# Kernel tuning notes

Hardware: AMD Instinct MI355X
Metric: run time of the kernel (lower is better)

## Reference

```python
import jax, jax.numpy as jnp
import numpy as np

H, W = 72, 128            # raster_h, raster_w
THICK = 0.03              # raster_thickness
SHARP = 80.0              # sigmoid sharpness
NRS = 64                  # match_resample_n
BIG = 1e9                 # finite stand-in for inf (grad-safe)
PTS_W, TAN_W, CURV_W, OVL_W = 5.0, 1.0, 0.5, 2.0


def _grid_xy():
    ys = jnp.linspace(0.0, 1.0, H)
    xs = jnp.linspace(0.0, 1.0, W)
    yy, xx = jnp.meshgrid(ys, xs, indexing='ij')
    return jnp.stack([xx, yy], -1).reshape(-1, 2)  # [H*W, 2]


def _prepare_mask(vis):
    # visibility -> per-point mask; curves with <2 visible points fall back to all-visible
    raw = vis > 0.5
    fallback = raw.sum(-1) < 2
    return jnp.where(fallback[:, None], 1.0, raw.astype(jnp.float32))  # [m, p]


def _resample(curves, pm, num):
    # arc-length resampling of [m, p, 2] polylines to [m, num, 2]
    m, p, _ = curves.shape
    seg_valid = pm[:, :-1] * pm[:, 1:]
    seg_len = jnp.linalg.norm(curves[:, 1:] - curves[:, :-1], axis=-1) * seg_valid
    cum = jnp.concatenate([jnp.zeros((m, 1), curves.dtype), jnp.cumsum(seg_len, -1)], -1)  # [m, p]
    total = cum[:, -1]
    base_t = jnp.linspace(0.0, 1.0, num)
    t = base_t[None] * total[:, None]  # [m, num]
    idx = jax.vmap(lambda c, tt: jnp.searchsorted(c, tt, side='right'))(cum, t) - 1
    idx = jnp.clip(idx, 0, p - 2)
    left = jnp.take_along_axis(curves[:, :-1], idx[..., None], axis=1)
    right = jnp.take_along_axis(curves[:, 1:], idx[..., None], axis=1)
    lt = jnp.take_along_axis(cum[:, :-1], idx, axis=1)
    rt = jnp.take_along_axis(cum[:, 1:], idx, axis=1)
    alpha = ((t - lt) / jnp.maximum(rt - lt, 1e-8))[..., None]
    out = left + alpha * (right - left)
    return jnp.where((total < 1e-8)[:, None, None], curves[:, :1, :], out)


def _tangents(pts):
    # central-difference unit tangents, [m, n, 2]
    fwd = jnp.concatenate([pts[:, 1:2] - pts[:, 0:1],
                           pts[:, 2:] - pts[:, :-2],
                           pts[:, -1:] - pts[:, -2:-1]], axis=1)
    return fwd / jnp.maximum(jnp.linalg.norm(fwd, axis=-1, keepdims=True), 1e-8)


def _pt2poly(A, B):
    # mean over resampled points of A of min point-to-segment distance to polyline B
    # A: [qa, r, 2], B: [qb, r, 2] -> [qa, qb]
    seg_a = B[:, :-1]
    ab = B[:, 1:] - seg_a
    denom = jnp.maximum((ab * ab).sum(-1), 1e-8)  # [qb, s]
    ap = A[:, None, :, None, :] - seg_a[None, :, None]           # [qa, qb, r, s, 2]
    t = jnp.clip((ap * ab[None, :, None]).sum(-1) / denom[None, :, None], 0.0, 1.0)
    proj = seg_a[None, :, None] + t[..., None] * ab[None, :, None]
    dist = jnp.linalg.norm(A[:, None, :, None, :] - proj, axis=-1)  # [qa, qb, r, s]
    return dist.min(-1).mean(-1)


def _smooth_l1(x, y):
    d = jnp.abs(x - y)
    return jnp.where(d < 1.0, 0.5 * d * d, d - 0.5)


def _soft_mask(curves, pm, grid):
    # soft rasterization of polylines: [m, p, 2] -> [m, H*W]
    seg_a = curves[:, :-1]
    ab = curves[:, 1:] - seg_a
    denom = jnp.maximum((ab * ab).sum(-1), 1e-8)          # [m, s]
    seg_valid = (pm[:, :-1] * pm[:, 1:]) > 0.5
    ap = grid[None, :, None, :] - seg_a[:, None]          # [m, HW, s, 2]
    t = jnp.clip((ap * ab[:, None]).sum(-1) / denom[:, None], 0.0, 1.0)
    proj = seg_a[:, None] + t[..., None] * ab[:, None]
    dist = jnp.linalg.norm(grid[None, :, None, :] - proj, axis=-1)  # [m, HW, s]
    dist = jnp.where(seg_valid[:, None], dist, BIG)
    min_dist = dist.min(-1)
    # fallback to nearest visible point when a curve has no valid segment
    no_valid = ~seg_valid.any(-1)
    pd = jnp.linalg.norm(grid[None, :, None, :] - curves[:, None], axis=-1)  # [m, HW, p]
    pd = jnp.where(pm[:, None] > 0.5, pd, BIG)
    min_dist = jnp.where(no_valid[:, None], pd.min(-1), min_dist)
    return jax.nn.sigmoid((THICK - min_dist) * SHARP)


def _cost_single(pred, gtp, gtv, grid):
    gt_pm = _prepare_mask(gtv)
    ones_pm = jnp.ones(pred.shape[:2], pred.dtype)
    pred_rs = _resample(pred, ones_pm, NRS)
    gt_rs = _resample(gtp, gt_pm, NRS)
    d_pg = _pt2poly(pred_rs, gt_rs)
    d_gp = _pt2poly(gt_rs, pred_rs).T
    sym = 0.5 * (d_pg + d_gp)                                   # [Q, M]
    pt = _tangents(pred_rs)
    gt_t = _tangents(gt_rs)
    tan = 1.0 - jnp.abs((pt[:, None] * gt_t[None]).sum(-1)).mean(-1)
    ps = pred_rs[:, 2:] - 2 * pred_rs[:, 1:-1] + pred_rs[:, :-2]
    gs = gt_rs[:, 2:] - 2 * gt_rs[:, 1:-1] + gt_rs[:, :-2]
    curv = _smooth_l1(ps[:, None], gs[None]).mean((-1, -2))
    pmask = _soft_mask(pred, ones_pm, grid)                     # [Q, HW]
    gmask = _soft_mask(gtp, gt_pm, grid)                        # [M, HW]
    inter = jnp.minimum(pmask[:, None], gmask[None]).sum(-1)
    union = jnp.maximum(pmask[:, None], gmask[None]).sum(-1)
    overlap = 1.0 - inter / (union + 1e-8)
    return PTS_W * sym + TAN_W * tan + CURV_W * curv + OVL_W * overlap


def setup_inputs() -> dict:
    key = jax.random.key(0)
    k1, k2, k3, k4 = jax.random.split(key, 4)
    return {
        'pred_pts': jax.random.uniform(k1, (2, 40, 24, 2), jnp.float32),
        'gt_pts': jax.random.uniform(k2, (2, 24, 24, 2), jnp.float32),
        'gt_vis': jax.random.uniform(k3, (2, 24, 24), jnp.float32),
        'gt_exist': jax.random.uniform(k4, (2, 24), jnp.float32),
    }


def reference(pred_pts, gt_pts, gt_vis, gt_exist):
    grid = _grid_xy()
    cost = jax.vmap(lambda p, g, v: _cost_single(p, g, v, grid))(pred_pts, gt_pts, gt_vis)
    # zero out columns for non-existent GT lanes (original skips them via boolean indexing)
    return cost * (gt_exist > 0.5).astype(cost.dtype)[:, None, :]  # [B, Q, M]
```

## Files before the change

### kernel.cpp

```cpp
#include <hip/hip_runtime.h>
#include <math.h>

#define Hh 72
#define Ww 128
#define HW (Hh*Ww)
#define NP 24
#define NSEG (NP-1)
#define Mp 40
#define Ng 24
#define Bb 2
#define NRS 64
#define THICKc 0.03f
#define SHARPc 80.0f

__global__ __launch_bounds__(64) void k_resample(
    const float* __restrict__ pred,
    const float* __restrict__ gt,
    const float* __restrict__ vis,
    float* __restrict__ predRS,
    float* __restrict__ gtRS,
    float* __restrict__ gtPM)
{
    int blk = blockIdx.x;
    int b = blk / (Mp + Ng);
    int c = blk % (Mp + Ng);
    bool isPred = (c < Mp);
    int tid = threadIdx.x;

    __shared__ float qx[NP], qy[NP], pm[NP], cum[NP];
    __shared__ float s_total;

    const float* src = isPred ? pred + (size_t)(b * Mp + c) * NP * 2
                              : gt   + (size_t)(b * Ng + (c - Mp)) * NP * 2;
    if (tid < NP) {
        float2 v = ((const float2*)src)[tid];
        qx[tid] = v.x;
        qy[tid] = v.y;
        pm[tid] = isPred ? 1.0f
                         : ((vis[(b * Ng + (c - Mp)) * NP + tid] > 0.5f) ? 1.0f : 0.0f);
    }
    __syncthreads();
    if (tid == 0) {
        if (!isPred) {
            float s = 0.0f;
            for (int p = 0; p < NP; p++) s += pm[p];
            if (s < 2.0f)
                for (int p = 0; p < NP; p++) pm[p] = 1.0f;
        }
        float acc = 0.0f;
        cum[0] = 0.0f;
        for (int s = 0; s < NSEG; s++) {
            float dx = qx[s + 1] - qx[s], dy = qy[s + 1] - qy[s];
            float sl = sqrtf(dx * dx + dy * dy) * (pm[s] * pm[s + 1]);
            acc += sl;
            cum[s + 1] = acc;
        }
        s_total = acc;
    }
    __syncthreads();
    if (!isPred && tid < NP) gtPM[(b * Ng + (c - Mp)) * NP + tid] = pm[tid];

    float total = s_total;
    float t = ((float)tid / 63.0f) * total;
    int cnt = 0;
    for (int p = 0; p < NP; p++) cnt += (cum[p] <= t) ? 1 : 0;
    int idx = cnt - 1;
    idx = (idx < 0) ? 0 : ((idx > NP - 2) ? NP - 2 : idx);
    float lt = cum[idx], rt = cum[idx + 1];
    float alpha = (t - lt) / fmaxf(rt - lt, 1e-8f);
    float ox = qx[idx] + alpha * (qx[idx + 1] - qx[idx]);
    float oy = qy[idx] + alpha * (qy[idx + 1] - qy[idx]);
    if (total < 1e-8f) { ox = qx[0]; oy = qy[0]; }
    float* dst = isPred ? predRS + (size_t)(b * Mp + c) * NRS * 2
                        : gtRS   + (size_t)(b * Ng + (c - Mp)) * NRS * 2;
    dst[tid * 2 + 0] = ox;
    dst[tid * 2 + 1] = oy;
}

__global__ __launch_bounds__(256) void k_softmask(
    const float* __restrict__ pred,
    const float* __restrict__ gt,
    const float* __restrict__ gtPM,
    float* __restrict__ pmask,
    float* __restrict__ gmask)
{
    int c = blockIdx.y;
    int b = c / (Mp + Ng);
    int cc = c % (Mp + Ng);
    bool isPred = (cc < Mp);
    int g = blockIdx.x * blockDim.x + threadIdx.x;

    __shared__ float qx[NP], qy[NP], pm[NP];
    __shared__ float sax[NSEG], say[NSEG], sabx[NSEG], saby[NSEG], sinv[NSEG], svld[NSEG];
    if (threadIdx.x < NP) {
        const float* src = isPred ? pred + (size_t)(b * Mp + cc) * NP * 2
                                  : gt   + (size_t)(b * Ng + (cc - Mp)) * NP * 2;
        float2 v = ((const float2*)src)[threadIdx.x];
        qx[threadIdx.x] = v.x;
        qy[threadIdx.x] = v.y;
        pm[threadIdx.x] = isPred ? 1.0f : gtPM[(b * Ng + (cc - Mp)) * NP + threadIdx.x];
    }
    __syncthreads();
    if (threadIdx.x < NSEG) {
        int s = threadIdx.x;
        float ax = qx[s], ay = qy[s];
        float abx = qx[s + 1] - ax, aby = qy[s + 1] - ay;
        sax[s] = ax; say[s] = ay; sabx[s] = abx; saby[s] = aby;
        sinv[s] = 1.0f / fmaxf(abx * abx + aby * aby, 1e-8f);
        svld[s] = (pm[s] * pm[s + 1] > 0.5f) ? 1.0f : 0.0f;
    }
    __syncthreads();

    float gx = (float)(g & (Ww - 1)) * (1.0f / 127.0f);
    float gy = (float)(g >> 7) * (1.0f / 71.0f);

    float best2 = 1e30f;
    bool anyValid = false;
    for (int s = 0; s < NSEG; s++) {
        if (svld[s] > 0.5f) {
            anyValid = true;
            float ax = sax[s], ay = say[s];
            float abx = sabx[s], aby = saby[s];
            float t = ((gx - ax) * abx + (gy - ay) * aby) * sinv[s];
            t = fminf(fmaxf(t, 0.0f), 1.0f);
            float dx = gx - (ax + t * abx), dy = gy - (ay + t * aby);
            best2 = fminf(best2, dx * dx + dy * dy);
        }
    }
    float mind;
    if (anyValid) {
        mind = sqrtf(best2);
    } else {
        float b2 = 1e30f;
        for (int p = 0; p < NP; p++) {
            if (pm[p] > 0.5f) {
                float dx = gx - qx[p], dy = gy - qy[p];
                b2 = fminf(b2, dx * dx + dy * dy);
            }
        }
        mind = sqrtf(b2);
    }
    float x = (THICKc - mind) * SHARPc;
    float mval = 1.0f / (1.0f + __expf(-x));
    if (isPred) pmask[(size_t)(b * Mp + cc) * HW + g] = mval;
    else        gmask[(size_t)(b * Ng + (cc - Mp)) * HW + g] = mval;
}

__global__ __launch_bounds__(256) void k_cost(
    const float* __restrict__ predRS,
    const float* __restrict__ gtRS,
    const float* __restrict__ pmask,
    const float* __restrict__ gmask,
    const float* __restrict__ gtExist,
    float* __restrict__ out)
{
    int pair = blockIdx.x;
    int j = pair % Ng;
    int i = (pair / Ng) % Mp;
    int b = pair / (Ng * Mp);
    int tid = threadIdx.x;
    int lane = tid & 63, wid = tid >> 6;

    __shared__ float px[NRS], py[NRS], gxr[NRS], gyr[NRS];
    __shared__ float pmin[4], psp[4], psq[4];

    if (tid < NRS) {
        px[tid]  = predRS[((size_t)(b * Mp + i) * NRS + tid) * 2 + 0];
        py[tid]  = predRS[((size_t)(b * Mp + i) * NRS + tid) * 2 + 1];
        gxr[tid] = gtRS[((size_t)(b * Ng + j) * NRS + tid) * 2 + 0];
        gyr[tid] = gtRS[((size_t)(b * Ng + j) * NRS + tid) * 2 + 1];
    }
    __syncthreads();

    const float4* pm4 = (const float4*)(pmask + (size_t)(b * Mp + i) * HW);
    const float4* gm4 = (const float4*)(gmask + (size_t)(b * Ng + j) * HW);
    float smin = 0.0f, sp = 0.0f, sq = 0.0f;
    for (int g = tid; g < HW / 4; g += 256) {
        float4 p = pm4[g], q = gm4[g];
        smin += fminf(p.x, q.x) + fminf(p.y, q.y) + fminf(p.z, q.z) + fminf(p.w, q.w);
        sp   += p.x + p.y + p.z + p.w;
        sq   += q.x + q.y + q.z + q.w;
    }

    float symv = 0.0f, tanv = 0.0f, curvv = 0.0f;
    if (wid == 0) {
        float p0x = px[lane], p0y = py[lane];
        float bst = 1e30f;
        for (int s = 0; s < NRS - 1; s++) {
            float ax = gxr[s], ay = gyr[s];
            float abx = gxr[s + 1] - ax, aby = gyr[s + 1] - ay;
            float denom = fmaxf(abx * abx + aby * aby, 1e-8f);
            float t = ((p0x - ax) * abx + (p0y - ay) * aby) / denom;
            t = fminf(fmaxf(t, 0.0f), 1.0f);
            float dx = p0x - (ax + t * abx), dy = p0y - (ay + t * aby);
            bst = fminf(bst, dx * dx + dy * dy);
        }
        float dpg = sqrtf(bst);
        float q0x = gxr[lane], q0y = gyr[lane];
        bst = 1e30f;
        for (int s = 0; s < NRS - 1; s++) {
            float ax = px[s], ay = py[s];
            float abx = px[s + 1] - ax, aby = py[s + 1] - ay;
            float denom = fmaxf(abx * abx + aby * aby, 1e-8f);
            float t = ((q0x - ax) * abx + (q0y - ay) * aby) / denom;
            t = fminf(fmaxf(t, 0.0f), 1.0f);
            float dx = q0x - (ax + t * abx), dy = q0y - (ay + t * aby);
            bst = fminf(bst, dx * dx + dy * dy);
        }
        float dgp = sqrtf(bst);
        symv = 0.5f * (dpg + dgp);

        int kp = (lane == NRS - 1) ? NRS - 1 : lane + 1;
        int km = (lane == 0) ? 0 : lane - 1;
        float tx = px[kp] - px[km], ty = py[kp] - py[km];
        float nrm = fmaxf(sqrtf(tx * tx + ty * ty), 1e-8f);
        tx /= nrm; ty /= nrm;
        float gtx = gxr[kp] - gxr[km], gty = gyr[kp] - gyr[km];
        float nrm2 = fmaxf(sqrtf(gtx * gtx + gty * gty), 1e-8f);
        gtx /= nrm2; gty /= nrm2;
        tanv = fabsf(tx * gtx + ty * gty);

        if (lane < NRS - 2) {
            float psx = px[lane + 2] - 2.0f * px[lane + 1] + px[lane];
            float psy = py[lane + 2] - 2.0f * py[lane + 1] + py[lane];
            float gsx = gxr[lane + 2] - 2.0f * gxr[lane + 1] + gxr[lane];
            float gsy = gyr[lane + 2] - 2.0f * gyr[lane + 1] + gyr[lane];
            float d1 = fabsf(psx - gsx);
            float d2 = fabsf(psy - gsy);
            float c1 = (d1 < 1.0f) ? 0.5f * d1 * d1 : d1 - 0.5f;
            float c2 = (d2 < 1.0f) ? 0.5f * d2 * d2 : d2 - 0.5f;
            curvv = c1 + c2;
        }
    }

    for (int off = 32; off > 0; off >>= 1) {
        smin += __shfl_down(smin, off);
        sp   += __shfl_down(sp, off);
        sq   += __shfl_down(sq, off);
    }
    if (lane == 0) { pmin[wid] = smin; psp[wid] = sp; psq[wid] = sq; }
    if (wid == 0) {
        for (int off = 32; off > 0; off >>= 1) {
            symv  += __shfl_down(symv,  off);
            tanv  += __shfl_down(tanv,  off);
            curvv += __shfl_down(curvv, off);
        }
    }
    __syncthreads();

    if (tid == 0) {
        float Smin = pmin[0] + pmin[1] + pmin[2] + pmin[3];
        float Sp   = psp[0] + psp[1] + psp[2] + psp[3];
        float Sq   = psq[0] + psq[1] + psq[2] + psq[3];
        float Smax = Sp + Sq - Smin;
        float overlap = 1.0f - Smin / (Smax + 1e-8f);
        float sym  = symv * (1.0f / 64.0f);
        float tanl = 1.0f - tanv * (1.0f / 64.0f);
        float curv = curvv * (1.0f / 124.0f);
        float cost = 5.0f * sym + 1.0f * tanl + 0.5f * curv + 2.0f * overlap;
        float e = (gtExist[b * Ng + j] > 0.5f) ? 1.0f : 0.0f;
        out[(size_t)(b * Mp + i) * Ng + j] = cost * e;
    }
}

extern "C" void kernel_launch(void* const* d_in, const int* in_sizes, int n_in,
                              void* d_out, int out_size, void* d_ws, size_t ws_size,
                              hipStream_t stream) {
    (void)in_sizes; (void)n_in; (void)out_size; (void)ws_size;
    const float* pred  = (const float*)d_in[0];
    const float* gt    = (const float*)d_in[1];
    const float* vis   = (const float*)d_in[2];
    const float* exist = (const float*)d_in[3];

    float* ws      = (float*)d_ws;
    float* predRS  = ws;
    float* gtRS    = predRS + (size_t)Bb * Mp * NRS * 2;
    float* gtPM    = gtRS   + (size_t)Bb * Ng * NRS * 2;
    float* pmask   = gtPM   + (size_t)Bb * Ng * NP;
    float* gmask   = pmask  + (size_t)Bb * Mp * HW;
    float* outp    = (float*)d_out;

    hipLaunchKernelGGL(k_resample, dim3(Bb * (Mp + Ng)), dim3(64), 0, stream,
                       pred, gt, vis, predRS, gtRS, gtPM);
    hipLaunchKernelGGL(k_softmask, dim3(HW / 256, Bb * (Mp + Ng)), dim3(256), 0, stream,
                       pred, gt, gtPM, pmask, gmask);
    hipLaunchKernelGGL(k_cost, dim3(Bb * Mp * Ng), dim3(256), 0, stream,
                       predRS, gtRS, pmask, gmask, exist, outp);
}
```

Measured before the change: 99.71 us.

## Precompute compacted segment data and tile cost kernel over 2x2 pred/GT pairs

The prep kernel now builds a compacted list of valid segments per curve, with the projection coefficients already folded in. The soft-mask kernel then loops only over those segments using FMAs and no branches. The cost kernel handles a 2x2 tile of (pred, GT) pairs per block, so each mask row is loaded once and reused for two intersections. The chamfer, tangent and curvature terms are spread across all four waves instead of one. This cuts global mask traffic, but each block now does more register-heavy work and there are fewer blocks (480 instead of 1920).

Measured after the change: 100.8 us. Within noise of the previous version (+1.0%).

```diff
diff --git a/kernel.cpp b/kernel.cpp
--- a/kernel.cpp
+++ b/kernel.cpp
@@ -12,32 +12,35 @@
 #define NRS 64
 #define THICKc 0.03f
 #define SHARPc 80.0f
-
-__global__ __launch_bounds__(64) void k_resample(
+#define NCURV (Bb*(Mp+Ng))
+
+__global__ __launch_bounds__(64) void k_prep(
     const float* __restrict__ pred,
     const float* __restrict__ gt,
     const float* __restrict__ vis,
     float* __restrict__ predRS,
     float* __restrict__ gtRS,
-    float* __restrict__ gtPM)
+    float* __restrict__ segData,
+    int*   __restrict__ segCount)
 {
-    int blk = blockIdx.x;
-    int b = blk / (Mp + Ng);
-    int c = blk % (Mp + Ng);
-    bool isPred = (c < Mp);
+    int c = blockIdx.x;
+    bool isPred = (c < Bb * Mp);
+    int b   = isPred ? (c / Mp) : ((c - Bb * Mp) / Ng);
+    int idx = isPred ? (c % Mp) : ((c - Bb * Mp) % Ng);
+    const float* src = isPred ? pred + (size_t)(b * Mp + idx) * NP * 2
+                              : gt   + (size_t)(b * Ng + idx) * NP * 2;
     int tid = threadIdx.x;
 
     __shared__ float qx[NP], qy[NP], pm[NP], cum[NP];
+    __shared__ int   sidx[NP];
+    __shared__ int   s_mode;
     __shared__ float s_total;
 
-    const float* src = isPred ? pred + (size_t)(b * Mp + c) * NP * 2
-                              : gt   + (size_t)(b * Ng + (c - Mp)) * NP * 2;
     if (tid < NP) {
         float2 v = ((const float2*)src)[tid];
-        qx[tid] = v.x;
-        qy[tid] = v.y;
+        qx[tid] = v.x; qy[tid] = v.y;
         pm[tid] = isPred ? 1.0f
-                         : ((vis[(b * Ng + (c - Mp)) * NP + tid] > 0.5f) ? 1.0f : 0.0f);
+                         : ((vis[(b * Ng + idx) * NP + tid] > 0.5f) ? 1.0f : 0.0f);
     }
     __syncthreads();
     if (tid == 0) {
@@ -51,215 +54,216 @@
         cum[0] = 0.0f;
         for (int s = 0; s < NSEG; s++) {
             float dx = qx[s + 1] - qx[s], dy = qy[s + 1] - qy[s];
-            float sl = sqrtf(dx * dx + dy * dy) * (pm[s] * pm[s + 1]);
-            acc += sl;
+            acc += sqrtf(dx * dx + dy * dy) * (pm[s] * pm[s + 1]);
             cum[s + 1] = acc;
         }
         s_total = acc;
-    }
-    __syncthreads();
-    if (!isPred && tid < NP) gtPM[(b * Ng + (c - Mp)) * NP + tid] = pm[tid];
+        int n = 0;
+        for (int s = 0; s < NSEG; s++) sidx[s] = (pm[s] * pm[s + 1] > 0.5f) ? n++ : -1;
+        if (n > 0) {
+            s_mode = 0;
+        } else {
+            s_mode = 1;
+            for (int p = 0; p < NP; p++) sidx[p] = (pm[p] > 0.5f) ? n++ : -1;
+        }
+        segCount[c] = n;
+    }
+    __syncthreads();
+
+    if (s_mode == 0) {
+        if (tid < NSEG && sidx[tid] >= 0) {
+            float ax = qx[tid], ay = qy[tid];
+            float abx = qx[tid + 1] - ax, aby = qy[tid + 1] - ay;
+            float inv = 1.0f / fmaxf(abx * abx + aby * aby, 1e-8f);
+            float* r = segData + ((size_t)c * NP + sidx[tid]) * 8;
+            r[0] = ax;  r[1] = ay;  r[2] = abx;       r[3] = aby;
+            r[4] = abx * inv; r[5] = aby * inv; r[6] = (ax * abx + ay * aby) * inv; r[7] = 0.f;
+        }
+    } else {
+        if (tid < NP && sidx[tid] >= 0) {
+            float* r = segData + ((size_t)c * NP + sidx[tid]) * 8;
+            r[0] = qx[tid]; r[1] = qy[tid]; r[2] = 0.f; r[3] = 0.f;
+            r[4] = 0.f;     r[5] = 0.f;     r[6] = 0.f; r[7] = 0.f;
+        }
+    }
 
     float total = s_total;
     float t = ((float)tid / 63.0f) * total;
     int cnt = 0;
     for (int p = 0; p < NP; p++) cnt += (cum[p] <= t) ? 1 : 0;
-    int idx = cnt - 1;
-    idx = (idx < 0) ? 0 : ((idx > NP - 2) ? NP - 2 : idx);
-    float lt = cum[idx], rt = cum[idx + 1];
+    int id2 = cnt - 1;
+    id2 = (id2 < 0) ? 0 : ((id2 > NP - 2) ? NP - 2 : id2);
+    float lt = cum[id2], rt = cum[id2 + 1];
     float alpha = (t - lt) / fmaxf(rt - lt, 1e-8f);
-    float ox = qx[idx] + alpha * (qx[idx + 1] - qx[idx]);
-    float oy = qy[idx] + alpha * (qy[idx + 1] - qy[idx]);
+    float ox = qx[id2] + alpha * (qx[id2 + 1] - qx[id2]);
+    float oy = qy[id2] + alpha * (qy[id2 + 1] - qy[id2]);
     if (total < 1e-8f) { ox = qx[0]; oy = qy[0]; }
-    float* dst = isPred ? predRS + (size_t)(b * Mp + c) * NRS * 2
-                        : gtRS   + (size_t)(b * Ng + (c - Mp)) * NRS * 2;
-    dst[tid * 2 + 0] = ox;
-    dst[tid * 2 + 1] = oy;
+    float* dst = isPred ? predRS + ((size_t)(b * Mp + idx) * NRS + tid) * 2
+                        : gtRS   + ((size_t)(b * Ng + idx) * NRS + tid) * 2;
+    dst[0] = ox; dst[1] = oy;
 }
 
 __global__ __launch_bounds__(256) void k_softmask(
-    const float* __restrict__ pred,
-    const float* __restrict__ gt,
-    const float* __restrict__ gtPM,
-    float* __restrict__ pmask,
-    float* __restrict__ gmask)
+    const float* __restrict__ segData,
+    const int*   __restrict__ segCount,
+    float* __restrict__ maskAll)
 {
     int c = blockIdx.y;
-    int b = c / (Mp + Ng);
-    int cc = c % (Mp + Ng);
-    bool isPred = (cc < Mp);
-    int g = blockIdx.x * blockDim.x + threadIdx.x;
-
-    __shared__ float qx[NP], qy[NP], pm[NP];
-    __shared__ float sax[NSEG], say[NSEG], sabx[NSEG], saby[NSEG], sinv[NSEG], svld[NSEG];
-    if (threadIdx.x < NP) {
-        const float* src = isPred ? pred + (size_t)(b * Mp + cc) * NP * 2
-                                  : gt   + (size_t)(b * Ng + (cc - Mp)) * NP * 2;
-        float2 v = ((const float2*)src)[threadIdx.x];
-        qx[threadIdx.x] = v.x;
-        qy[threadIdx.x] = v.y;
-        pm[threadIdx.x] = isPred ? 1.0f : gtPM[(b * Ng + (cc - Mp)) * NP + threadIdx.x];
-    }
-    __syncthreads();
-    if (threadIdx.x < NSEG) {
-        int s = threadIdx.x;
-        float ax = qx[s], ay = qy[s];
-        float abx = qx[s + 1] - ax, aby = qy[s + 1] - ay;
-        sax[s] = ax; say[s] = ay; sabx[s] = abx; saby[s] = aby;
-        sinv[s] = 1.0f / fmaxf(abx * abx + aby * aby, 1e-8f);
-        svld[s] = (pm[s] * pm[s + 1] > 0.5f) ? 1.0f : 0.0f;
-    }
-    __syncthreads();
+    int g = blockIdx.x * 256 + threadIdx.x;
+    int n = segCount[c];
+    const float4* sd = (const float4*)(segData + (size_t)c * NP * 8);
 
     float gx = (float)(g & (Ww - 1)) * (1.0f / 127.0f);
-    float gy = (float)(g >> 7) * (1.0f / 71.0f);
+    float gy = (float)(g >> 7)       * (1.0f / 71.0f);
 
     float best2 = 1e30f;
-    bool anyValid = false;
-    for (int s = 0; s < NSEG; s++) {
-        if (svld[s] > 0.5f) {
-            anyValid = true;
-            float ax = sax[s], ay = say[s];
-            float abx = sabx[s], aby = saby[s];
-            float t = ((gx - ax) * abx + (gy - ay) * aby) * sinv[s];
-            t = fminf(fmaxf(t, 0.0f), 1.0f);
-            float dx = gx - (ax + t * abx), dy = gy - (ay + t * aby);
-            best2 = fminf(best2, dx * dx + dy * dy);
-        }
-    }
-    float mind;
-    if (anyValid) {
-        mind = sqrtf(best2);
-    } else {
-        float b2 = 1e30f;
-        for (int p = 0; p < NP; p++) {
-            if (pm[p] > 0.5f) {
-                float dx = gx - qx[p], dy = gy - qy[p];
-                b2 = fminf(b2, dx * dx + dy * dy);
-            }
-        }
-        mind = sqrtf(b2);
-    }
-    float x = (THICKc - mind) * SHARPc;
-    float mval = 1.0f / (1.0f + __expf(-x));
-    if (isPred) pmask[(size_t)(b * Mp + cc) * HW + g] = mval;
-    else        gmask[(size_t)(b * Ng + (cc - Mp)) * HW + g] = mval;
+    for (int s = 0; s < n; s++) {
+        float4 A  = sd[s * 2];
+        float4 Bv = sd[s * 2 + 1];
+        float t = fmaf(gx, Bv.x, fmaf(gy, Bv.y, -Bv.z));
+        t = fminf(fmaxf(t, 0.0f), 1.0f);
+        float dx = gx - fmaf(t, A.z, A.x);
+        float dy = gy - fmaf(t, A.w, A.y);
+        best2 = fminf(best2, fmaf(dx, dx, dy * dy));
+    }
+    float mind = sqrtf(best2);
+    float mval = 1.0f / (1.0f + __expf((mind - THICKc) * SHARPc));
+    maskAll[(size_t)c * HW + g] = mval;
 }
 
 __global__ __launch_bounds__(256) void k_cost(
     const float* __restrict__ predRS,
     const float* __restrict__ gtRS,
-    const float* __restrict__ pmask,
-    const float* __restrict__ gmask,
+    const float* __restrict__ maskAll,
     const float* __restrict__ gtExist,
     float* __restrict__ out)
 {
-    int pair = blockIdx.x;
-    int j = pair % Ng;
-    int i = (pair / Ng) % Mp;
-    int b = pair / (Ng * Mp);
+    int blk = blockIdx.x;
+    int tj = blk % 12;
+    int ti = (blk / 12) % 20;
+    int b  = blk / (12 * 20);
+    int i0 = ti * 2, j0 = tj * 2;
     int tid = threadIdx.x;
-    int lane = tid & 63, wid = tid >> 6;
-
-    __shared__ float px[NRS], py[NRS], gxr[NRS], gyr[NRS];
-    __shared__ float pmin[4], psp[4], psq[4];
-
-    if (tid < NRS) {
-        px[tid]  = predRS[((size_t)(b * Mp + i) * NRS + tid) * 2 + 0];
-        py[tid]  = predRS[((size_t)(b * Mp + i) * NRS + tid) * 2 + 1];
-        gxr[tid] = gtRS[((size_t)(b * Ng + j) * NRS + tid) * 2 + 0];
-        gyr[tid] = gtRS[((size_t)(b * Ng + j) * NRS + tid) * 2 + 1];
-    }
-    __syncthreads();
-
-    const float4* pm4 = (const float4*)(pmask + (size_t)(b * Mp + i) * HW);
-    const float4* gm4 = (const float4*)(gmask + (size_t)(b * Ng + j) * HW);
-    float smin = 0.0f, sp = 0.0f, sq = 0.0f;
+    int lane = tid & 63, w = tid >> 6;
+
+    __shared__ float sPx[2][NRS], sPy[2][NRS], sGx[2][NRS], sGy[2][NRS];
+    __shared__ float partA[4][8];
+    __shared__ float cham[4][3];
+
+    {
+        int ci = tid >> 6, pt = tid & 63;
+        if (ci < 2) {
+            float2 v = ((const float2*)predRS)[(b * Mp + i0 + ci) * NRS + pt];
+            sPx[ci][pt] = v.x; sPy[ci][pt] = v.y;
+        } else {
+            int cj = ci - 2;
+            float2 v = ((const float2*)gtRS)[(b * Ng + j0 + cj) * NRS + pt];
+            sGx[cj][pt] = v.x; sGy[cj][pt] = v.y;
+        }
+    }
+    __syncthreads();
+
+    const float4* P0 = (const float4*)(maskAll + (size_t)(b * Mp + i0)     * HW);
+    const float4* P1 = (const float4*)(maskAll + (size_t)(b * Mp + i0 + 1) * HW);
+    const float4* Q0 = (const float4*)(maskAll + (size_t)(Bb * Mp + b * Ng + j0)     * HW);
+    const float4* Q1 = (const float4*)(maskAll + (size_t)(Bb * Mp + b * Ng + j0 + 1) * HW);
+    float sm00 = 0, sm01 = 0, sm10 = 0, sm11 = 0;
+    float sp0 = 0, sp1 = 0, sq0 = 0, sq1 = 0;
     for (int g = tid; g < HW / 4; g += 256) {
-        float4 p = pm4[g], q = gm4[g];
-        smin += fminf(p.x, q.x) + fminf(p.y, q.y) + fminf(p.z, q.z) + fminf(p.w, q.w);
-        sp   += p.x + p.y + p.z + p.w;
-        sq   += q.x + q.y + q.z + q.w;
-    }
-
-    float symv = 0.0f, tanv = 0.0f, curvv = 0.0f;
-    if (wid == 0) {
-        float p0x = px[lane], p0y = py[lane];
-        float bst = 1e30f;
+        float4 p0 = P0[g], p1 = P1[g], q0 = Q0[g], q1 = Q1[g];
+        sp0 += p0.x + p0.y + p0.z + p0.w;
+        sp1 += p1.x + p1.y + p1.z + p1.w;
+        sq0 += q0.x + q0.y + q0.z + q0.w;
+        sq1 += q1.x + q1.y + q1.z + q1.w;
+        sm00 += fminf(p0.x,q0.x) + fminf(p0.y,q0.y) + fminf(p0.z,q0.z) + fminf(p0.w,q0.w);
+        sm01 += fminf(p0.x,q1.x) + fminf(p0.y,q1.y) + fminf(p0.z,q1.z) + fminf(p0.w,q1.w);
+        sm10 += fminf(p1.x,q0.x) + fminf(p1.y,q0.y) + fminf(p1.z,q0.z) + fminf(p1.w,q0.w);
+        sm11 += fminf(p1.x,q1.x) + fminf(p1.y,q1.y) + fminf(p1.z,q1.z) + fminf(p1.w,q1.w);
+    }
+    for (int off = 32; off > 0; off >>= 1) {
+        sm00 += __shfl_down(sm00, off); sm01 += __shfl_down(sm01, off);
+        sm10 += __shfl_down(sm10, off); sm11 += __shfl_down(sm11, off);
+        sp0  += __shfl_down(sp0,  off); sp1  += __shfl_down(sp1,  off);
+        sq0  += __shfl_down(sq0,  off); sq1  += __shfl_down(sq1,  off);
+    }
+    if (lane == 0) {
+        partA[w][0] = sm00; partA[w][1] = sm01; partA[w][2] = sm10; partA[w][3] = sm11;
+        partA[w][4] = sp0;  partA[w][5] = sp1;  partA[w][6] = sq0;  partA[w][7] = sq1;
+    }
+
+    {
+        int a = w >> 1, cj = w & 1;
+        const float* PX = sPx[a];  const float* PY = sPy[a];
+        const float* GX = sGx[cj]; const float* GY = sGy[cj];
+        float p0x = PX[lane], p0y = PY[lane];
+        float q0x = GX[lane], q0y = GY[lane];
+        float b1 = 1e30f, b2 = 1e30f;
         for (int s = 0; s < NRS - 1; s++) {
-            float ax = gxr[s], ay = gyr[s];
-            float abx = gxr[s + 1] - ax, aby = gyr[s + 1] - ay;
-            float denom = fmaxf(abx * abx + aby * aby, 1e-8f);
-            float t = ((p0x - ax) * abx + (p0y - ay) * aby) / denom;
-            t = fminf(fmaxf(t, 0.0f), 1.0f);
-            float dx = p0x - (ax + t * abx), dy = p0y - (ay + t * aby);
-            bst = fminf(bst, dx * dx + dy * dy);
-        }
-        float dpg = sqrtf(bst);
-        float q0x = gxr[lane], q0y = gyr[lane];
-        bst = 1e30f;
-        for (int s = 0; s < NRS - 1; s++) {
-            float ax = px[s], ay = py[s];
-            float abx = px[s + 1] - ax, aby = py[s + 1] - ay;
-            float denom = fmaxf(abx * abx + aby * aby, 1e-8f);
-            float t = ((q0x - ax) * abx + (q0y - ay) * aby) / denom;
-            t = fminf(fmaxf(t, 0.0f), 1.0f);
-            float dx = q0x - (ax + t * abx), dy = q0y - (ay + t * aby);
-            bst = fminf(bst, dx * dx + dy * dy);
-        }
-        float dgp = sqrtf(bst);
-        symv = 0.5f * (dpg + dgp);
+            {
+                float ax = GX[s], ay = GY[s];
+                float abx = GX[s + 1] - ax, aby = GY[s + 1] - ay;
+                float denom = fmaxf(abx * abx + aby * aby, 1e-8f);
+                float t = ((p0x - ax) * abx + (p0y - ay) * aby) / denom;
+                t = fminf(fmaxf(t, 0.0f), 1.0f);
+                float dx = p0x - (ax + t * abx), dy = p0y - (ay + t * aby);
+                b1 = fminf(b1, dx * dx + dy * dy);
+            }
+            {
+                float ax = PX[s], ay = PY[s];
+                float abx = PX[s + 1] - ax, aby = PY[s + 1] - ay;
+                float denom = fmaxf(abx * abx + aby * aby, 1e-8f);
+                float t = ((q0x - ax) * abx + (q0y - ay) * aby) / denom;
+                t = fminf(fmaxf(t, 0.0f), 1.0f);
+                float dx = q0x - (ax + t * abx), dy = q0y - (ay + t * aby);
+                b2 = fminf(b2, dx * dx + dy * dy);
+            }
+        }
+        float symv = 0.5f * (sqrtf(b1) + sqrtf(b2));
 
         int kp = (lane == NRS - 1) ? NRS - 1 : lane + 1;
         int km = (lane == 0) ? 0 : lane - 1;
-        float tx = px[kp] - px[km], ty = py[kp] - py[km];
+        float tx = PX[kp] - PX[km], ty = PY[kp] - PY[km];
         float nrm = fmaxf(sqrtf(tx * tx + ty * ty), 1e-8f);
         tx /= nrm; ty /= nrm;
-        float gtx = gxr[kp] - gxr[km], gty = gyr[kp] - gyr[km];
+        float gtx = GX[kp] - GX[km], gty = GY[kp] - GY[km];
         float nrm2 = fmaxf(sqrtf(gtx * gtx + gty * gty), 1e-8f);
         gtx /= nrm2; gty /= nrm2;
-        tanv = fabsf(tx * gtx + ty * gty);
-
+        float tanv = fabsf(tx * gtx + ty * gty);
+
+        float curvv = 0.0f;
         if (lane < NRS - 2) {
-            float psx = px[lane + 2] - 2.0f * px[lane + 1] + px[lane];
-            float psy = py[lane + 2] - 2.0f * py[lane + 1] + py[lane];
-            float gsx = gxr[lane + 2] - 2.0f * gxr[lane + 1] + gxr[lane];
-            float gsy = gyr[lane + 2] - 2.0f * gyr[lane + 1] + gyr[lane];
+            float psx = PX[lane + 2] - 2.0f * PX[lane + 1] + PX[lane];
+            float psy = PY[lane + 2] - 2.0f * PY[lane + 1] + PY[lane];
+            float gsx = GX[lane + 2] - 2.0f * GX[lane + 1] + GX[lane];
+            float gsy = GY[lane + 2] - 2.0f * GY[lane + 1] + GY[lane];
             float d1 = fabsf(psx - gsx);
             float d2 = fabsf(psy - gsy);
             float c1 = (d1 < 1.0f) ? 0.5f * d1 * d1 : d1 - 0.5f;
             float c2 = (d2 < 1.0f) ? 0.5f * d2 * d2 : d2 - 0.5f;
             curvv = c1 + c2;
         }
-    }
-
-    for (int off = 32; off > 0; off >>= 1) {
-        smin += __shfl_down(smin, off);
-        sp   += __shfl_down(sp, off);
-        sq   += __shfl_down(sq, off);
-    }
-    if (lane == 0) { pmin[wid] = smin; psp[wid] = sp; psq[wid] = sq; }
-    if (wid == 0) {
         for (int off = 32; off > 0; off >>= 1) {
             symv  += __shfl_down(symv,  off);
             tanv  += __shfl_down(tanv,  off);
             curvv += __shfl_down(curvv, off);
         }
-    }
-    __syncthreads();
-
-    if (tid == 0) {
-        float Smin = pmin[0] + pmin[1] + pmin[2] + pmin[3];
-        float Sp   = psp[0] + psp[1] + psp[2] + psp[3];
-        float Sq   = psq[0] + psq[1] + psq[2] + psq[3];
+        if (lane == 0) { cham[w][0] = symv; cham[w][1] = tanv; cham[w][2] = curvv; }
+    }
+    __syncthreads();
+
+    if (tid < 4) {
+        int a2 = tid >> 1, c2 = tid & 1;
+        float Smin = partA[0][tid] + partA[1][tid] + partA[2][tid] + partA[3][tid];
+        float Sp = partA[0][4 + a2] + partA[1][4 + a2] + partA[2][4 + a2] + partA[3][4 + a2];
+        float Sq = partA[0][6 + c2] + partA[1][6 + c2] + partA[2][6 + c2] + partA[3][6 + c2];
         float Smax = Sp + Sq - Smin;
         float overlap = 1.0f - Smin / (Smax + 1e-8f);
-        float sym  = symv * (1.0f / 64.0f);
-        float tanl = 1.0f - tanv * (1.0f / 64.0f);
-        float curv = curvv * (1.0f / 124.0f);
+        float sym  = cham[tid][0] * (1.0f / 64.0f);
+        float tanl = 1.0f - cham[tid][1] * (1.0f / 64.0f);
+        float curv = cham[tid][2] * (1.0f / 124.0f);
         float cost = 5.0f * sym + 1.0f * tanl + 0.5f * curv + 2.0f * overlap;
-        float e = (gtExist[b * Ng + j] > 0.5f) ? 1.0f : 0.0f;
-        out[(size_t)(b * Mp + i) * Ng + j] = cost * e;
+        float e = (gtExist[b * Ng + j0 + c2] > 0.5f) ? 1.0f : 0.0f;
+        out[(size_t)(b * Mp + i0 + a2) * Ng + j0 + c2] = cost * e;
     }
 }
 
@@ -275,15 +279,15 @@
     float* ws      = (float*)d_ws;
     float* predRS  = ws;
     float* gtRS    = predRS + (size_t)Bb * Mp * NRS * 2;
-    float* gtPM    = gtRS   + (size_t)Bb * Ng * NRS * 2;
-    float* pmask   = gtPM   + (size_t)Bb * Ng * NP;
-    float* gmask   = pmask  + (size_t)Bb * Mp * HW;
+    float* segData = gtRS   + (size_t)Bb * Ng * NRS * 2;
+    int*   segCount= (int*)(segData + (size_t)NCURV * NP * 8);
+    float* maskAll = (float*)(segCount + 128);
     float* outp    = (float*)d_out;
 
-    hipLaunchKernelGGL(k_resample, dim3(Bb * (Mp + Ng)), dim3(64), 0, stream,
-                       pred, gt, vis, predRS, gtRS, gtPM);
-    hipLaunchKernelGGL(k_softmask, dim3(HW / 256, Bb * (Mp + Ng)), dim3(256), 0, stream,
-                       pred, gt, gtPM, pmask, gmask);
-    hipLaunchKernelGGL(k_cost, dim3(Bb * Mp * Ng), dim3(256), 0, stream,
-                       predRS, gtRS, pmask, gmask, exist, outp);
-}
+    hipLaunchKernelGGL(k_prep, dim3(NCURV), dim3(64), 0, stream,
+                       pred, gt, vis, predRS, gtRS, segData, segCount);
+    hipLaunchKernelGGL(k_softmask, dim3(HW / 256, NCURV), dim3(256), 0, stream,
+                       segData, segCount, maskAll);
+    hipLaunchKernelGGL(k_cost, dim3(Bb * 20 * 12), dim3(256), 0, stream,
+                       predRS, gtRS, maskAll, exist, outp);
+}
```
